# Performance work log

Measured on AMD Instinct MI355X. Metric: run time of the kernel, lower is better.

## Reference

```python
import jax, jax.numpy as jnp
import numpy as np

D_MODEL = 1024
NUM_HEADS = 16
HEAD_DIM = D_MODEL // NUM_HEADS


def setup_inputs() -> dict:
    key = jax.random.key(0)
    k_x, k_wqkv, k_bqkv, k_wo, k_bo = jax.random.split(key, 5)
    x = jax.random.normal(k_x, (2, 2048, D_MODEL), dtype=jnp.float32)
    s = 1.0 / np.sqrt(D_MODEL)
    W_qkv = jax.random.uniform(k_wqkv, (D_MODEL, 3 * D_MODEL), jnp.float32, -s, s)
    b_qkv = jax.random.uniform(k_bqkv, (3 * D_MODEL,), jnp.float32, -s, s)
    W_o = jax.random.uniform(k_wo, (D_MODEL, D_MODEL), jnp.float32, -s, s)
    b_o = jax.random.uniform(k_bo, (D_MODEL,), jnp.float32, -s, s)
    return {"x": x, "W_qkv": W_qkv, "b_qkv": b_qkv, "W_o": W_o, "b_o": b_o}


def reference(x, W_qkv, b_qkv, W_o, b_o):
    B, S, D = x.shape
    # fused QKV projection: [B,S,3D]
    qkv = jnp.einsum('bsd,de->bse', x, W_qkv) + b_qkv
    # [B,S,H,3*hd] -> [B,H,S,3*hd]
    qkv = qkv.reshape(B, S, NUM_HEADS, 3 * HEAD_DIM).transpose(0, 2, 1, 3)
    q, k, v = jnp.split(qkv, 3, axis=-1)  # each [B,H,S,hd]
    scale = 1.0 / jnp.sqrt(jnp.asarray(HEAD_DIM, dtype=x.dtype))
    scores = jnp.einsum('bhqd,bhkd->bhqk', q, k) * scale  # [B,H,S,S]
    attn = jax.nn.softmax(scores, axis=-1)
    values = jnp.einsum('bhqk,bhkd->bhqd', attn, v)  # [B,H,S,hd]
    values = values.transpose(0, 2, 1, 3).reshape(B, S, D)
    out = jnp.einsum('bsd,de->bse', values, W_o) + b_o
    return out
```

## Files before the change

### kernel.cpp

```cpp
#include <hip/hip_runtime.h>
#include <stdint.h>
#include <stddef.h>

typedef _Float16 f16;
typedef _Float16 f16x8 __attribute__((ext_vector_type(8)));
typedef _Float16 f16x4 __attribute__((ext_vector_type(4)));
typedef float    f32x2 __attribute__((ext_vector_type(2)));
typedef float    f32x4 __attribute__((ext_vector_type(4)));
typedef float    f32x16 __attribute__((ext_vector_type(16)));
typedef int      i32x4 __attribute__((ext_vector_type(4)));
typedef int      i32x2 __attribute__((ext_vector_type(2)));

#define S_LEN 2048
#define DM    1024
#define NH    16
#define HD    64
#define NTOK  4096
#define NQKV  3072
#define QSCALE 0.18033688011112042f

#if __has_builtin(__builtin_amdgcn_exp2f)
#define EXP2(x) __builtin_amdgcn_exp2f(x)
#else
#define EXP2(x) __expf((x) * 0.69314718055994531f)
#endif

__device__ __forceinline__ void gl_lds16(const void* g, void* l) {
  __builtin_amdgcn_global_load_lds(
      (const __attribute__((address_space(1))) void*)g,
      (__attribute__((address_space(3))) void*)l, 16, 0, 0);
}

__device__ __forceinline__ void pl32_swap(int& a, int& b) {
#if __has_builtin(__builtin_amdgcn_permlane32_swap)
  i32x2 r = __builtin_amdgcn_permlane32_swap(a, b, false, false);
  a = r.x; b = r.y;
#else
  asm volatile("v_permlane32_swap_b32 %0, %1" : "+v"(a), "+v"(b));
#endif
}

__device__ __forceinline__ float swap_half(float x, int hi) {
  int a = __builtin_bit_cast(int, x);
  int b = a;
  pl32_swap(a, b);
  return __builtin_bit_cast(float, hi ? a : b);
}

__device__ __forceinline__ int pkrtz(float a, float b) {
  auto h = __builtin_amdgcn_cvt_pkrtz(a, b);
  return __builtin_bit_cast(int, h);
}

__device__ __forceinline__ f16x8 mk_frag(int a, int b, int c, int d) {
  i32x4 v = {a, b, c, d};
  return __builtin_bit_cast(f16x8, v);
}

__device__ __forceinline__ f32x2 pk2(const f32x16& v, int i) {
  f32x2 r = {v[2*i], v[2*i+1]};
  return r;
}

__global__ __launch_bounds__(256) void cvt_all_kernel(
    const float* __restrict__ x,    f16* __restrict__ x_h,
    const float* __restrict__ Wqkv, f16* __restrict__ Wqkv_t,
    const float* __restrict__ Wo,   f16* __restrict__ Wo_t)
{
  __shared__ float t[32][33];
  const int b = blockIdx.x, tid = threadIdx.x;
  if (b < 2048) {
    int i = (b * 256 + tid) * 8;
    float4 a0 = *(const float4*)(x + i);
    float4 a1 = *(const float4*)(x + i + 4);
    f16x8 v = {(f16)a0.x,(f16)a0.y,(f16)a0.z,(f16)a0.w,(f16)a1.x,(f16)a1.y,(f16)a1.z,(f16)a1.w};
    *(f16x8*)(x_h + i) = v;
    return;
  }
  const float* in; f16* out; int R, C, c0, r0;
  if (b < 5120) {
    int tt = b - 2048; in = Wqkv; out = Wqkv_t; R = DM; C = NQKV;
    c0 = (tt % 96) * 32; r0 = (tt / 96) * 32;
  } else {
    int tt = b - 5120; in = Wo; out = Wo_t; R = DM; C = DM;
    c0 = (tt & 31) * 32; r0 = (tt >> 5) * 32;
  }
  int tx = tid & 31, ty = tid >> 5;
  #pragma unroll
  for (int i = 0; i < 4; ++i)
    t[ty + i*8][tx] = in[(size_t)(r0 + ty + i*8) * C + c0 + tx];
  __syncthreads();
  #pragma unroll
  for (int i = 0; i < 4; ++i)
    out[(size_t)(c0 + ty + i*8) * R + r0 + tx] = (f16)t[tx][ty + i*8];
}

__global__ __launch_bounds__(256) void gemm_qkv_kernel(
    const f16* __restrict__ A, const f16* __restrict__ Bt,
    const float* __restrict__ bias,
    f16* __restrict__ qb, f16* __restrict__ kb, f16* __restrict__ vtb)
{
  __shared__ f16 As[128*32];
  __shared__ f16 Bs[128*32];
  const int tid = threadIdx.x;
  const int wid = tid >> 6, lane = tid & 63;
  const int g = lane >> 4, r = lane & 15;
  const int flat = blockIdx.x;
  const int xcd = flat & 7, idx = flat >> 3;
  const int m0 = (xcd * 4 + (idx & 3)) * 128;
  const int n0 = (idx >> 2) * 128;
  const int wm = (wid >> 1) * 64, wn = (wid & 1) * 64;

  f32x4 acc[4][4] = {};
  const int srow = tid >> 2;
  const int sch  = tid & 3;

  for (int kt = 0; kt < DM/32; ++kt) {
    const int k0 = kt * 32;
    __syncthreads();
    #pragma unroll
    for (int c = 0; c < 2; ++c) {
      int row = c*64 + srow;
      int sw = (sch ^ ((row >> 1) & 3)) * 8;
      gl_lds16(A  + (size_t)(m0 + row) * DM + k0 + sw, (char*)As + c*4096 + tid*16);
      gl_lds16(Bt + (size_t)(n0 + row) * DM + k0 + sw, (char*)Bs + c*4096 + tid*16);
    }
    __syncthreads();
    f16x8 a[4], b[4];
    #pragma unroll
    for (int mt = 0; mt < 4; ++mt) {
      int rl = wm + mt*16 + r;
      a[mt] = *(const f16x8*)(As + rl*32 + ((g ^ ((rl >> 1) & 3)) * 8));
    }
    #pragma unroll
    for (int nt = 0; nt < 4; ++nt) {
      int cl = wn + nt*16 + r;
      b[nt] = *(const f16x8*)(Bs + cl*32 + ((g ^ ((cl >> 1) & 3)) * 8));
    }
    #pragma unroll
    for (int mt = 0; mt < 4; ++mt)
      #pragma unroll
      for (int nt = 0; nt < 4; ++nt)
        acc[mt][nt] = __builtin_amdgcn_mfma_f32_16x16x32_f16(a[mt], b[nt], acc[mt][nt], 0, 0, 0);
  }

  #pragma unroll
  for (int mt = 0; mt < 4; ++mt) {
    int row0 = m0 + wm + mt*16 + g*4;
    int b_ = row0 >> 11, s0 = row0 & 2047;
    #pragma unroll
    for (int nt = 0; nt < 4; ++nt) {
      int col = n0 + wn + nt*16 + r;
      float bv = bias[col];
      int h = col / 192;
      int cc = col - h*192;
      int which = cc >> 6, d = cc & 63;
      size_t bh = (size_t)(b_*NH + h);
      if (which == 2) {
        f16x4 v;
        #pragma unroll
        for (int i = 0; i < 4; ++i) v[i] = (f16)(acc[mt][nt][i] + bv);
        *(f16x4*)(vtb + (bh*HD + d)*S_LEN + s0) = v;
      } else if (which == 0) {
        #pragma unroll
        for (int i = 0; i < 4; ++i)
          qb[(bh*S_LEN + s0 + i)*HD + d] = (f16)((acc[mt][nt][i] + bv) * QSCALE);
      } else {
        #pragma unroll
        for (int i = 0; i < 4; ++i)
          kb[(bh*S_LEN + s0 + i)*HD + d] = (f16)(acc[mt][nt][i] + bv);
      }
    }
  }
}

__global__ __launch_bounds__(256) void gemm_out_kernel(
    const f16* __restrict__ A, const f16* __restrict__ Bt,
    const float* __restrict__ bias, float* __restrict__ out)
{
  __shared__ f16 As[128*32];
  __shared__ f16 Bs[64*32];
  const int tid = threadIdx.x;
  const int wid = tid >> 6, lane = tid & 63;
  const int g = lane >> 4, r = lane & 15;
  const int flat = blockIdx.x;
  const int xcd = flat & 7, idx = flat >> 3;
  const int m0 = (xcd * 4 + (idx & 3)) * 128;
  const int n0 = (idx >> 2) * 64;
  const int wm = (wid >> 1) * 64, wn = (wid & 1) * 32;

  f32x4 acc[4][2] = {};
  const int srowA = tid >> 2, schA = tid & 3;
  const int prB = tid >> 2,  pcB = tid & 3;
  const int lcB = pcB ^ ((prB >> 1) & 3);

  for (int kt = 0; kt < DM/32; ++kt) {
    const int k0 = kt * 32;
    __syncthreads();
    #pragma unroll
    for (int c = 0; c < 2; ++c) {
      int row = c*64 + srowA;
      int sw = (schA ^ ((row >> 1) & 3)) * 8;
      gl_lds16(A + (size_t)(m0 + row) * DM + k0 + sw, (char*)As + c*4096 + tid*16);
    }
    gl_lds16(Bt + (size_t)(n0 + prB) * DM + k0 + lcB*8, (char*)Bs + tid*16);
    __syncthreads();
    f16x8 a[4], b[2];
    #pragma unroll
    for (int mt = 0; mt < 4; ++mt) {
      int rl = wm + mt*16 + r;
      a[mt] = *(const f16x8*)(As + rl*32 + ((g ^ ((rl >> 1) & 3)) * 8));
    }
    #pragma unroll
    for (int nt = 0; nt < 2; ++nt) {
      int cl = wn + nt*16 + r;
      b[nt] = *(const f16x8*)(Bs + cl*32 + ((g ^ ((cl >> 1) & 3)) * 8));
    }
    #pragma unroll
    for (int mt = 0; mt < 4; ++mt)
      #pragma unroll
      for (int nt = 0; nt < 2; ++nt)
        acc[mt][nt] = __builtin_amdgcn_mfma_f32_16x16x32_f16(a[mt], b[nt], acc[mt][nt], 0, 0, 0);
  }

  #pragma unroll
  for (int mt = 0; mt < 4; ++mt) {
    int row0 = m0 + wm + mt*16 + g*4;
    #pragma unroll
    for (int nt = 0; nt < 2; ++nt) {
      int col = n0 + wn + nt*16 + r;
      float bv = bias[col];
      #pragma unroll
      for (int i = 0; i < 4; ++i)
        out[(size_t)(row0 + i)*DM + col] = acc[mt][nt][i] + bv;
    }
  }
}

__global__ __launch_bounds__(512) void attn_kernel(
    const f16* __restrict__ qb, const f16* __restrict__ kb,
    const f16* __restrict__ vtb, f16* __restrict__ values)
{
  __shared__ __align__(16) char smem[67584];

  const int tid = threadIdx.x;
  const int wid = tid >> 6, lane = tid & 63;
  const int wq = wid & 3, wk = wid >> 2;
  const int ql = lane & 31, hi = lane >> 5;
  const int flat = blockIdx.x;
  const int xcd = flat & 7, idx = flat >> 3;
  const int bh = xcd * 4 + (idx & 3);
  const int q0 = (idx >> 2) * 256 + wq * 64;
  const f16* qh = qb  + (size_t)bh * S_LEN * HD;
  const f16* kh = kb  + (size_t)bh * S_LEN * HD;
  const f16* vh = vtb + (size_t)bh * HD * S_LEN;
  const int kbase0 = wk * 1024;
  const int htid = tid & 255;

  int koff[2], voff[2];
  #pragma unroll
  for (int c = 0; c < 2; ++c) {
    int ca = htid + c*256, pr = ca >> 4, pc = ca & 15, lc = pc ^ (pr & 15);
    int row2 = pr*2 + (lc >> 3), e8 = (lc & 7) * 8;
    koff[c] = row2 * HD + e8;
    voff[c] = row2 * S_LEN + e8;
  }

  f16x8 qfA[4], qfB[4];
  #pragma unroll
  for (int dk = 0; dk < 4; ++dk) {
    qfA[dk] = *(const f16x8*)(qh + (size_t)(q0 + ql)*HD + dk*16 + hi*8);
    qfB[dk] = *(const f16x8*)(qh + (size_t)(q0 + 32 + ql)*HD + dk*16 + hi*8);
  }

  const int r0b = (ql >> 1) << 8;
  const int xv  = (ql >> 1) & 15;
  const int hb  = ((ql & 1) << 3) | hi;

  f32x2 laccA = {0.f, 0.f}, laccB = {0.f, 0.f};
  f32x16 oA0 = {}, oA1 = {}, oB0 = {}, oB1 = {};
  f32x16 sA0, sA1, sB0, sB1;
  const f32x16 ZERO = {};

  #define STAGE(kt_, buf_) do {                                            \
    const f16* ks_ = kh + (size_t)(kbase0 + (kt_)*64) * HD;                \
    const f16* vs_ = vh + (kbase0 + (kt_)*64);                             \
    char* kd_ = smem + (wk*2 + (buf_))*8192;                               \
    char* vd_ = smem + 32768 + (wk*2 + (buf_))*8192;                       \
    gl_lds16(ks_ + koff[0], kd_ + htid*16);                                \
    gl_lds16(ks_ + koff[1], kd_ + 4096 + htid*16);                         \
    gl_lds16(vs_ + voff[0], vd_ + htid*16);                                \
    gl_lds16(vs_ + voff[1], vd_ + 4096 + htid*16);                         \
  } while (0)

  #define QK_STEP(buf_) do {                                               \
    const char* KsC = smem + (wk*2 + (buf_))*8192;                         \
    {                                                                      \
      int off0 = r0b + ((hb ^ xv) << 4);                                   \
      f16x8 kf0 = *(const f16x8*)(KsC + off0);                             \
      f16x8 kf1 = *(const f16x8*)(KsC + 4096 + off0);                      \
      sA0 = __builtin_amdgcn_mfma_f32_32x32x16_f16(kf0, qfA[0], ZERO, 0, 0, 0); \
      sB0 = __builtin_amdgcn_mfma_f32_32x32x16_f16(kf0, qfB[0], ZERO, 0, 0, 0); \
      sA1 = __builtin_amdgcn_mfma_f32_32x32x16_f16(kf1, qfA[0], ZERO, 0, 0, 0); \
      sB1 = __builtin_amdgcn_mfma_f32_32x32x16_f16(kf1, qfB[0], ZERO, 0, 0, 0); \
    }                                                                      \
    _Pragma("unroll")                                                      \
    for (int dk = 1; dk < 4; ++dk) {                                       \
      int off = r0b + (((hb | (dk << 1)) ^ xv) << 4);                      \
      f16x8 kf0 = *(const f16x8*)(KsC + off);                              \
      f16x8 kf1 = *(const f16x8*)(KsC + 4096 + off);                       \
      sA0 = __builtin_amdgcn_mfma_f32_32x32x16_f16(kf0, qfA[dk], sA0, 0, 0, 0); \
      sB0 = __builtin_amdgcn_mfma_f32_32x32x16_f16(kf0, qfB[dk], sB0, 0, 0, 0); \
      sA1 = __builtin_amdgcn_mfma_f32_32x32x16_f16(kf1, qfA[dk], sA1, 0, 0, 0); \
      sB1 = __builtin_amdgcn_mfma_f32_32x32x16_f16(kf1, qfB[dk], sB1, 0, 0, 0); \
    }                                                                      \
  } while (0)

  #define EXP_H(S_, LACC_, PFA_, PFB_) do {                                \
    _Pragma("unroll")                                                      \
    for (int i = 0; i < 16; ++i) S_[i] = EXP2(S_[i]);                      \
    f32x2 sm[4];                                                           \
    _Pragma("unroll")                                                      \
    for (int i = 0; i < 4; ++i) sm[i] = pk2(S_, i) + pk2(S_, i + 4);       \
    sm[0] += sm[1]; sm[2] += sm[3]; LACC_ += sm[0] + sm[2];                \
    int a = pkrtz(S_[0], S_[1]), b = pkrtz(S_[2], S_[3]);                  \
    int c = pkrtz(S_[4], S_[5]), d = pkrtz(S_[6], S_[7]);                  \
    pl32_swap(a, c); pl32_swap(b, d);                                      \
    PFA_ = mk_frag(a, b, c, d);                                            \
    a = pkrtz(S_[8],  S_[9]);  b = pkrtz(S_[10], S_[11]);                  \
    c = pkrtz(S_[12], S_[13]); d = pkrtz(S_[14], S_[15]);                  \
    pl32_swap(a, c); pl32_swap(b, d);                                      \
    PFB_ = mk_frag(a, b, c, d);                                            \
  } while (0)

  #define PV_STEP(buf_) do {                                               \
    const char* VsC = smem + 32768 + (wk*2 + (buf_))*8192;                 \
    _Pragma("unroll")                                                      \
    for (int w = 0; w < 4; ++w) {                                          \
      int off = r0b + (((hb | (w << 1)) ^ xv) << 4);                       \
      f16x8 vf0 = *(const f16x8*)(VsC + off);                              \
      f16x8 vf1 = *(const f16x8*)(VsC + 4096 + off);                       \
      oA0 = __builtin_amdgcn_mfma_f32_32x32x16_f16(pfA[w], vf0, oA0, 0, 0, 0); \
      oA1 = __builtin_amdgcn_mfma_f32_32x32x16_f16(pfA[w], vf1, oA1, 0, 0, 0); \
      oB0 = __builtin_amdgcn_mfma_f32_32x32x16_f16(pfB[w], vf0, oB0, 0, 0, 0); \
      oB1 = __builtin_amdgcn_mfma_f32_32x32x16_f16(pfB[w], vf1, oB1, 0, 0, 0); \
    }                                                                      \
  } while (0)

  f16x8 pfA[4], pfB[4];
  STAGE(0, 0);
  __syncthreads();

  for (int kt = 0; kt < 16; ++kt) {
    const int cur = kt & 1;
    if (kt + 1 < 16) STAGE(kt + 1, cur ^ 1);
    QK_STEP(cur);
    EXP_H(sA0, laccA, pfA[0], pfA[1]);
    EXP_H(sA1, laccA, pfA[2], pfA[3]);
    EXP_H(sB0, laccB, pfB[0], pfB[1]);
    EXP_H(sB1, laccB, pfB[2], pfB[3]);
    PV_STEP(cur);
    __syncthreads();
  }
  #undef STAGE
  #undef QK_STEP
  #undef EXP_H
  #undef PV_STEP

  float lA = laccA.x + laccA.y;  lA += swap_half(lA, hi);
  float lB = laccB.x + laccB.y;  lB += swap_half(lB, hi);

  const int slot = wq*64 + lane;
  float* lpl = (float*)(smem + 65536);
  float* ipl = (float*)(smem + 66560);
  if (wk == 1) {
    #pragma unroll
    for (int t = 0; t < 4; ++t) {
      *(f32x4*)(smem + (0*8 + 0*4 + t)*4096 + slot*16) = (f32x4){oA0[4*t], oA0[4*t+1], oA0[4*t+2], oA0[4*t+3]};
      *(f32x4*)(smem + (0*8 + 1*4 + t)*4096 + slot*16) = (f32x4){oA1[4*t], oA1[4*t+1], oA1[4*t+2], oA1[4*t+3]};
      *(f32x4*)(smem + (1*8 + 0*4 + t)*4096 + slot*16) = (f32x4){oB0[4*t], oB0[4*t+1], oB0[4*t+2], oB0[4*t+3]};
      *(f32x4*)(smem + (1*8 + 1*4 + t)*4096 + slot*16) = (f32x4){oB1[4*t], oB1[4*t+1], oB1[4*t+2], oB1[4*t+3]};
    }
    lpl[wq*64 + 0*32 + ql] = lA;
    lpl[wq*64 + 1*32 + ql] = lB;
  }
  __syncthreads();
  if (wk == 0) {
    float invA = 1.0f / (lA + lpl[wq*64 + ql]);
    float invB = 1.0f / (lB + lpl[wq*64 + 32 + ql]);
    ipl[wq*64 + ql]      = invA;
    ipl[wq*64 + 32 + ql] = invB;
  }
  __syncthreads();
  if (wk == 0) {
    const int b_ = bh >> 4, h = bh & 15;
    #pragma unroll
    for (int g2 = 0; g2 < 2; ++g2) {
      const f32x16& s0 = g2 ? oB0 : oA0;
      const f32x16& s1 = g2 ? oB1 : oA1;
      #pragma unroll
      for (int t = 0; t < 4; ++t) {
        f32x4 p0 = *(const f32x4*)(smem + (g2*8 + 0*4 + t)*4096 + slot*16);
        f32x4 p1 = *(const f32x4*)(smem + (g2*8 + 1*4 + t)*4096 + slot*16);
        f32x4 iv = *(const f32x4*)(ipl + wq*64 + g2*32 + 4*hi + 8*t);
        #pragma unroll
        for (int i = 0; i < 4; ++i) {
          int qrow = q0 + g2*32 + 4*hi + 8*t + i;
          size_t base = (size_t)(b_*S_LEN + qrow) * DM + h*HD + ql;
          values[base]      = (f16)((s0[4*t+i] + p0[i]) * iv[i]);
          values[base + 32] = (f16)((s1[4*t+i] + p1[i]) * iv[i]);
        }
      }
    }
  }
}

extern "C" void kernel_launch(void* const* d_in, const int* in_sizes, int n_in,
                              void* d_out, int out_size, void* d_ws, size_t ws_size,
                              hipStream_t stream) {
  (void)in_sizes; (void)n_in; (void)out_size; (void)ws_size;
  const float* x    = (const float*)d_in[0];
  const float* Wqkv = (const float*)d_in[1];
  const float* bqkv = (const float*)d_in[2];
  const float* Wo   = (const float*)d_in[3];
  const float* bo   = (const float*)d_in[4];
  float* out = (float*)d_out;

  char* ws = (char*)d_ws;
  f16* x_h    = (f16*)(ws);
  f16* Wqkv_t = (f16*)(ws + ( 8ull<<20));
  f16* Wo_t   = (f16*)(ws + (14ull<<20));
  f16* qbuf   = (f16*)(ws + (16ull<<20));
  f16* kbuf   = (f16*)(ws + (24ull<<20));
  f16* vtbuf  = (f16*)(ws + (32ull<<20));
  f16* vals   = (f16*)(ws + (40ull<<20));

  cvt_all_kernel<<<dim3(6144), dim3(256), 0, stream>>>(
      x, x_h, Wqkv, Wqkv_t, Wo, Wo_t);

  gemm_qkv_kernel<<<dim3(768), dim3(256), 0, stream>>>(
      x_h, Wqkv_t, bqkv, qbuf, kbuf, vtbuf);

  attn_kernel<<<dim3(256), dim3(512), 0, stream>>>(qbuf, kbuf, vtbuf, vals);

  gemm_out_kernel<<<dim3(512), dim3(256), 0, stream>>>(
      vals, Wo_t, bo, out);
}
```

Before: 105.1 us.

## Fuse x fp32-to-fp16 conversion into QKV GEMM tile loads

Drops the separate pass that converted x to fp16 and instead has the QKV GEMM load fp32 tiles of x directly into LDS with an XOR swizzle, converting to fp16 when building the MFMA fragments. This removes one full read and write of the activation tensor plus part of a kernel launch. In exchange the A-tile traffic per k-step doubles, since x is re-read in fp32 by each of the N-tile blocks. LDS use and per-iteration conversion work also grow.

```diff
diff --git a/kernel.cpp b/kernel.cpp
--- a/kernel.cpp
+++ b/kernel.cpp
@@ -62,27 +62,18 @@
   return r;
 }
 
-__global__ __launch_bounds__(256) void cvt_all_kernel(
-    const float* __restrict__ x,    f16* __restrict__ x_h,
+__global__ __launch_bounds__(256) void cvt_w_kernel(
     const float* __restrict__ Wqkv, f16* __restrict__ Wqkv_t,
     const float* __restrict__ Wo,   f16* __restrict__ Wo_t)
 {
   __shared__ float t[32][33];
   const int b = blockIdx.x, tid = threadIdx.x;
-  if (b < 2048) {
-    int i = (b * 256 + tid) * 8;
-    float4 a0 = *(const float4*)(x + i);
-    float4 a1 = *(const float4*)(x + i + 4);
-    f16x8 v = {(f16)a0.x,(f16)a0.y,(f16)a0.z,(f16)a0.w,(f16)a1.x,(f16)a1.y,(f16)a1.z,(f16)a1.w};
-    *(f16x8*)(x_h + i) = v;
-    return;
-  }
   const float* in; f16* out; int R, C, c0, r0;
-  if (b < 5120) {
-    int tt = b - 2048; in = Wqkv; out = Wqkv_t; R = DM; C = NQKV;
-    c0 = (tt % 96) * 32; r0 = (tt / 96) * 32;
+  if (b < 3072) {
+    in = Wqkv; out = Wqkv_t; R = DM; C = NQKV;
+    c0 = (b % 96) * 32; r0 = (b / 96) * 32;
   } else {
-    int tt = b - 5120; in = Wo; out = Wo_t; R = DM; C = DM;
+    int tt = b - 3072; in = Wo; out = Wo_t; R = DM; C = DM;
     c0 = (tt & 31) * 32; r0 = (tt >> 5) * 32;
   }
   int tx = tid & 31, ty = tid >> 5;
@@ -96,12 +87,12 @@
 }
 
 __global__ __launch_bounds__(256) void gemm_qkv_kernel(
-    const f16* __restrict__ A, const f16* __restrict__ Bt,
+    const float* __restrict__ A, const f16* __restrict__ Bt,
     const float* __restrict__ bias,
     f16* __restrict__ qb, f16* __restrict__ kb, f16* __restrict__ vtb)
 {
-  __shared__ f16 As[128*32];
-  __shared__ f16 Bs[128*32];
+  __shared__ __align__(16) float Asf[128*32];
+  __shared__ __align__(16) f16  Bs[128*32];
   const int tid = threadIdx.x;
   const int wid = tid >> 6, lane = tid & 63;
   const int g = lane >> 4, r = lane & 15;
@@ -112,6 +103,12 @@
   const int wm = (wid >> 1) * 64, wn = (wid & 1) * 64;
 
   f32x4 acc[4][4] = {};
+  int aoff[4];
+  #pragma unroll
+  for (int c = 0; c < 4; ++c) {
+    int ca = tid + c*256, pr = ca >> 3, pc = ca & 7, lc = pc ^ (pr & 7);
+    aoff[c] = pr * DM + lc * 4;
+  }
   const int srow = tid >> 2;
   const int sch  = tid & 3;
 
@@ -119,10 +116,12 @@
     const int k0 = kt * 32;
     __syncthreads();
     #pragma unroll
+    for (int c = 0; c < 4; ++c)
+      gl_lds16(A + (size_t)m0 * DM + k0 + aoff[c], (char*)Asf + c*4096 + tid*16);
+    #pragma unroll
     for (int c = 0; c < 2; ++c) {
       int row = c*64 + srow;
       int sw = (sch ^ ((row >> 1) & 3)) * 8;
-      gl_lds16(A  + (size_t)(m0 + row) * DM + k0 + sw, (char*)As + c*4096 + tid*16);
       gl_lds16(Bt + (size_t)(n0 + row) * DM + k0 + sw, (char*)Bs + c*4096 + tid*16);
     }
     __syncthreads();
@@ -130,7 +129,12 @@
     #pragma unroll
     for (int mt = 0; mt < 4; ++mt) {
       int rl = wm + mt*16 + r;
-      a[mt] = *(const f16x8*)(As + rl*32 + ((g ^ ((rl >> 1) & 3)) * 8));
+      int xr = rl & 7;
+      f32x4 lo = *(const f32x4*)((const char*)Asf + rl*128 + ((( (g<<1)      ) ^ xr) << 4));
+      f32x4 hv = *(const f32x4*)((const char*)Asf + rl*128 + ((( (g<<1) | 1 ) ^ xr) << 4));
+      f16x8 af = {(f16)lo.x,(f16)lo.y,(f16)lo.z,(f16)lo.w,
+                  (f16)hv.x,(f16)hv.y,(f16)hv.z,(f16)hv.w};
+      a[mt] = af;
     }
     #pragma unroll
     for (int nt = 0; nt < 4; ++nt) {
@@ -427,7 +431,6 @@
   float* out = (float*)d_out;
 
   char* ws = (char*)d_ws;
-  f16* x_h    = (f16*)(ws);
   f16* Wqkv_t = (f16*)(ws + ( 8ull<<20));
   f16* Wo_t   = (f16*)(ws + (14ull<<20));
   f16* qbuf   = (f16*)(ws + (16ull<<20));
@@ -435,11 +438,10 @@
   f16* vtbuf  = (f16*)(ws + (32ull<<20));
   f16* vals   = (f16*)(ws + (40ull<<20));
 
-  cvt_all_kernel<<<dim3(6144), dim3(256), 0, stream>>>(
-      x, x_h, Wqkv, Wqkv_t, Wo, Wo_t);
+  cvt_w_kernel<<<dim3(4096), dim3(256), 0, stream>>>(Wqkv, Wqkv_t, Wo, Wo_t);
 
   gemm_qkv_kernel<<<dim3(768), dim3(256), 0, stream>>>(
-      x_h, Wqkv_t, bqkv, qbuf, kbuf, vtbuf);
+      x, Wqkv_t, bqkv, qbuf, kbuf, vtbuf);
 
   attn_kernel<<<dim3(256), dim3(512), 0, stream>>>(qbuf, kbuf, vtbuf, vals);
 
```

Result: slower. 107.9 us (+2.6%).
